# Performance work log

Hardware: AMD Instinct MI355X
Metric: run time of the kernel (lower is better)

The kernel has to match this reference:

```python
import jax, jax.numpy as jnp
import numpy as np

N, E = 50000, 800000
NI, NH, NO, NA = 64, 64, 64, 8
C_WEIGHT = 1.0


def psi(p):
    return jnp.sign(p) * jnp.log(jnp.abs(p) + 1.0)


def batchnorm(x, gamma, beta, eps=1e-5):
    # torch BatchNorm1d (training mode): biased variance over the batch dim
    mu = jnp.mean(x, axis=0)
    var = jnp.var(x, axis=0)
    return (x - mu) / jnp.sqrt(var + eps) * gamma + beta


def setup_inputs() -> dict:
    key = jax.random.key(0)
    ks = jax.random.split(key, 16)
    f32 = jnp.float32

    def w(k, shape, s):
        return jax.random.normal(k, shape, dtype=f32) * s

    inp = {}
    inp["h"] = jax.random.normal(ks[0], (N, NI), dtype=f32)
    inp["x"] = jax.random.normal(ks[1], (N, 4), dtype=f32)
    inp["edge_i"] = jax.random.randint(ks[2], (E,), 0, N)
    inp["edge_j"] = jax.random.randint(ks[3], (E,), 0, N)
    inp["node_attr"] = jax.random.normal(ks[4], (N, NA), dtype=f32)
    # phi_e: Linear(2*NI+2 -> NH, no bias), BN, ReLU, Linear(NH -> NH), ReLU
    inp["W_e1"] = w(ks[5], (2 * NI + 2, NH), 0.1)
    inp["g_e"] = jnp.ones((NH,), f32)
    inp["b_e"] = jnp.zeros((NH,), f32)
    inp["W_e2"] = w(ks[6], (NH, NH), 0.1)
    inp["b_e2"] = jnp.zeros((NH,), f32)
    # phi_m: Linear(NH -> 1), Sigmoid
    inp["W_m"] = w(ks[7], (NH, 1), 0.1)
    inp["b_m"] = jnp.zeros((1,), f32)
    # phi_x: Linear(NH -> NH), ReLU, Linear(NH -> 1, no bias, xavier gain=0.001)
    inp["W_x1"] = w(ks[8], (NH, NH), 0.1)
    inp["b_x1"] = jnp.zeros((NH,), f32)
    inp["W_x2"] = w(ks[9], (NH, 1), 0.0003)
    # phi_h: Linear(NH+NI+NA -> NH), BN, ReLU, Linear(NH -> NO)
    inp["W_h1"] = w(ks[10], (NH + NI + NA, NH), 0.1)
    inp["b_h1"] = jnp.zeros((NH,), f32)
    inp["g_h"] = jnp.ones((NH,), f32)
    inp["b_h"] = jnp.zeros((NH,), f32)
    inp["W_h2"] = w(ks[11], (NH, NO), 0.1)
    inp["b_h2"] = jnp.zeros((NO,), f32)
    return inp


def reference(h, x, edge_i, edge_j, node_attr,
              W_e1, g_e, b_e, W_e2, b_e2,
              W_m, b_m, W_x1, b_x1, W_x2,
              W_h1, b_h1, g_h, b_h, W_h2, b_h2):
    n_nodes = h.shape[0]
    xi = x[edge_i]            # [E, 4]
    xj = x[edge_j]            # [E, 4]
    x_diff = xi - xj
    # Minkowski norm / dot: 2*p0*q0 - sum(p*q)
    psq = x_diff * x_diff
    norms = psi(2.0 * psq[:, 0] - psq.sum(axis=-1))[:, None]   # [E,1]
    pq = xi * xj
    dots = psi(2.0 * pq[:, 0] - pq.sum(axis=-1))[:, None]      # [E,1]
    # m_model
    feat = jnp.concatenate([h[edge_i], h[edge_j], norms, dots], axis=1)  # [E, 2*NI+2]
    out = jax.nn.relu(batchnorm(feat @ W_e1, g_e, b_e))
    out = jax.nn.relu(out @ W_e2 + b_e2)
    w_gate = jax.nn.sigmoid(out @ W_m + b_m)
    m = out * w_gate                                            # [E, NH]
    # x_model
    phx = jax.nn.relu(m @ W_x1 + b_x1) @ W_x2                   # [E, 1]
    trans = jnp.clip(x_diff * phx, -100.0, 100.0)
    agg_x = jax.ops.segment_sum(trans, edge_i, num_segments=n_nodes)
    cnt = jax.ops.segment_sum(jnp.ones((trans.shape[0],), trans.dtype),
                              edge_i, num_segments=n_nodes)
    x_new = x + (agg_x / jnp.maximum(cnt, 1.0)[:, None]) * C_WEIGHT
    # h_model
    agg_h = jax.ops.segment_sum(m, edge_i, num_segments=n_nodes)
    hin = jnp.concatenate([h, agg_h, node_attr], axis=1)        # [N, NH+NI+NA]
    hh = jax.nn.relu(batchnorm(hin @ W_h1 + b_h1, g_h, b_h))
    h_new = h + (hh @ W_h2 + b_h2)
    return (h_new, x_new, m)
```

## Files before the change

kernel.cpp:

```cpp
#include <hip/hip_runtime.h>
#include <stdint.h>

typedef __attribute__((ext_vector_type(8))) short bf16x8;
typedef __attribute__((ext_vector_type(4))) float f32x4;

static constexpr int NN = 50000;
static constexpr int NE = 800000;

static constexpr int O_ESUM = 0;
static constexpr int O_ESQ  = 64;
static constexpr int O_HSUM = 128;
static constexpr int O_HSQ  = 192;
static constexpr int O_ESC  = 256;
static constexpr int O_ESH  = 320;
static constexpr int O_HSC  = 384;
static constexpr int O_HSH  = 448;
static constexpr int O_CNT  = 512;
static constexpr int O_ROW  = O_CNT + 50048;
static constexpr int O_CUR  = O_ROW + 50048;
static constexpr int O_BSUM = O_CUR + 50048;
static constexpr int O_CSR  = O_BSUM + 64;
static constexpr int O_PHX  = O_CSR + NE;
static constexpr int O_AGGH = O_PHX + NE;
static constexpr int O_YH   = O_AGGH + NN*64;
static constexpr int O_PQ   = O_YH + NN*64;
static constexpr int O_YB   = O_PQ + NN*64;
static constexpr int O_ND   = O_YB + NE*32;

static constexpr int OUT_X = NN*64;
static constexpr int OUT_M = NN*64 + NN*4;

__device__ __forceinline__ short f2bf(float f){
  uint32_t u = __builtin_bit_cast(uint32_t, f);
  u = (u + 0x7fffu + ((u >> 16) & 1u)) >> 16;
  return (short)u;
}
__device__ __forceinline__ float bflo(uint32_t w){ return __builtin_bit_cast(float, w << 16); }
__device__ __forceinline__ float bfhi(uint32_t w){ return __builtin_bit_cast(float, w & 0xffff0000u); }
__device__ __forceinline__ float psi_f(float p){
  return copysignf(__logf(fabsf(p) + 1.0f), p);
}
__device__ __forceinline__ bf16x8 ldrow8(const float* p){
  float4 p0 = *(const float4*)p;
  float4 p1 = *(const float4*)(p + 4);
  bf16x8 a;
  a[0]=f2bf(p0.x); a[1]=f2bf(p0.y); a[2]=f2bf(p0.z); a[3]=f2bf(p0.w);
  a[4]=f2bf(p1.x); a[5]=f2bf(p1.y); a[6]=f2bf(p1.z); a[7]=f2bf(p1.w);
  return a;
}

__global__ __launch_bounds__(256) void k_pq(
    const float* __restrict__ h, const float* __restrict__ We1,
    ushort* __restrict__ P, ushort* __restrict__ Q)
{
  __shared__ __align__(16) ushort sT[4][1024];
  const int lane = threadIdx.x & 63, wid = threadIdx.x >> 6;
  const int g = lane >> 4, q = lane & 15;
  const int ro = lane >> 2, cb = lane & 3;

  bf16x8 wt[2][4], wm[2][4];
#pragma unroll
  for (int kb=0;kb<2;kb++)
#pragma unroll
    for (int nb=0;nb<4;nb++)
#pragma unroll
      for (int j=0;j<8;j++){
        wt[kb][nb][j] = f2bf(We1[(32*kb + 8*g + j)*64 + 16*nb + q]);
        wm[kb][nb][j] = f2bf(We1[(64 + 32*kb + 8*g + j)*64 + 16*nb + q]);
      }

  ushort* tb = sT[wid];
  const int gw = blockIdx.x*4 + wid, nw = gridDim.x*4;
  for (int t = gw; t < NN/16; t += nw){
    const int rb = t*16;
    const float* hp = h + (size_t)(rb+q)*64;
    bf16x8 a[2];
    a[0] = ldrow8(hp + 8*g); a[1] = ldrow8(hp + 32 + 8*g);

    f32x4 accP[4], accQ[4];
#pragma unroll
    for (int nb=0;nb<4;nb++){ accP[nb] = (f32x4){0.f,0.f,0.f,0.f}; accQ[nb] = (f32x4){0.f,0.f,0.f,0.f}; }
#pragma unroll
    for (int kb=0;kb<2;kb++)
#pragma unroll
      for (int nb=0;nb<4;nb++){
        accP[nb] = __builtin_amdgcn_mfma_f32_16x16x32_bf16(a[kb], wt[kb][nb], accP[nb], 0,0,0);
        accQ[nb] = __builtin_amdgcn_mfma_f32_16x16x32_bf16(a[kb], wm[kb][nb], accQ[nb], 0,0,0);
      }

    asm volatile("s_waitcnt lgkmcnt(0)" ::: "memory");
#pragma unroll
    for (int nb=0;nb<4;nb++)
#pragma unroll
      for (int r=0;r<4;r++){
        const int mr = 4*g + r;
        tb[mr*64 + ((16*nb + q) ^ ((mr&7)<<3))] = (ushort)f2bf(accP[nb][r]);
      }
    asm volatile("s_waitcnt lgkmcnt(0)" ::: "memory");
    {
      const int s = ro & 7;
      uint4 c0 = *(const uint4*)(tb + ro*64 + ((cb*16    ) ^ (s<<3)));
      uint4 c1 = *(const uint4*)(tb + ro*64 + ((cb*16 + 8) ^ (s<<3)));
      *(uint4*)(P + (size_t)(rb+ro)*64 + cb*16    ) = c0;
      *(uint4*)(P + (size_t)(rb+ro)*64 + cb*16 + 8) = c1;
    }
    asm volatile("s_waitcnt lgkmcnt(0)" ::: "memory");
#pragma unroll
    for (int nb=0;nb<4;nb++)
#pragma unroll
      for (int r=0;r<4;r++){
        const int mr = 4*g + r;
        tb[mr*64 + ((16*nb + q) ^ ((mr&7)<<3))] = (ushort)f2bf(accQ[nb][r]);
      }
    asm volatile("s_waitcnt lgkmcnt(0)" ::: "memory");
    {
      const int s = ro & 7;
      uint4 c0 = *(const uint4*)(tb + ro*64 + ((cb*16    ) ^ (s<<3)));
      uint4 c1 = *(const uint4*)(tb + ro*64 + ((cb*16 + 8) ^ (s<<3)));
      *(uint4*)(Q + (size_t)(rb+ro)*64 + cb*16    ) = c0;
      *(uint4*)(Q + (size_t)(rb+ro)*64 + cb*16 + 8) = c1;
    }
  }
}

__global__ __launch_bounds__(256) void k_nd(
    const float* __restrict__ x,
    const int* __restrict__ ei, const int* __restrict__ ej,
    float2* __restrict__ nd, int* __restrict__ cnt)
{
  const int stride = gridDim.x*256;
  for (int e = blockIdx.x*256 + threadIdx.x; e < NE; e += stride){
    const int i = ei[e], j = ej[e];
    const float4 xi = *(const float4*)(x + 4*i);
    const float4 xj = *(const float4*)(x + 4*j);
    const float dx=xi.x-xj.x, dy=xi.y-xj.y, dz=xi.z-xj.z, dw=xi.w-xj.w;
    float2 v;
    v.x = psi_f(dx*dx - dy*dy - dz*dz - dw*dw);
    v.y = psi_f(xi.x*xj.x - xi.y*xj.y - xi.z*xj.z - xi.w*xj.w);
    nd[e] = v;
    atomicAdd(cnt + i, 1);
  }
}

__global__ __launch_bounds__(256) void k_e1(
    const ushort* __restrict__ P, const ushort* __restrict__ Q,
    const int* __restrict__ ei, const int* __restrict__ ej,
    const float2* __restrict__ nd,
    const float* __restrict__ We1,
    ushort* __restrict__ yb, float* __restrict__ wsf)
{
  __shared__ float sred[8][64];
  const int lane = threadIdx.x & 63, wid = threadIdx.x >> 6;
  const float wn = We1[128*64 + lane];
  const float wd = We1[129*64 + lane];
  float ssum = 0.f, ssq = 0.f;

  const int gw = blockIdx.x*4 + wid, nw = gridDim.x*4;
  for (int t = gw; t < NE/8; t += nw){
    const int eb = __builtin_amdgcn_readfirstlane(t*8);
    int iv[8], jv[8];
    float nr[8], dt[8];
#pragma unroll
    for (int k=0;k<8;k++){
      iv[k] = ei[eb+k];
      jv[k] = ej[eb+k];
      const float2 v = nd[eb+k];
      nr[k] = v.x; dt[k] = v.y;
    }
    uint32_t pv[8], qv[8];
#pragma unroll
    for (int k=0;k<8;k++) pv[k] = P[(size_t)iv[k]*64 + lane];
#pragma unroll
    for (int k=0;k<8;k++) qv[k] = Q[(size_t)jv[k]*64 + lane];
#pragma unroll
    for (int k=0;k<8;k++){
      const float y = bflo(pv[k]) + bflo(qv[k]) + nr[k]*wn + dt[k]*wd;
      ssum += y; ssq += y*y;
      yb[(size_t)(eb+k)*64 + lane] = (ushort)f2bf(y);
    }
  }
  sred[wid][lane] = ssum;
  sred[4+wid][lane] = ssq;
  __syncthreads();
  if (wid == 0){
    const float s = sred[0][lane]+sred[1][lane]+sred[2][lane]+sred[3][lane];
    const float z = sred[4][lane]+sred[5][lane]+sred[6][lane]+sred[7][lane];
    atomicAdd(wsf + O_ESUM + lane, s);
    atomicAdd(wsf + O_ESQ  + lane, z);
  }
}

__global__ void k_stats(const float* __restrict__ sum, const float* __restrict__ sq,
                        const float* __restrict__ gam, const float* __restrict__ bet,
                        float* __restrict__ scale, float* __restrict__ shift, float invc){
  int t = threadIdx.x;
  float mu = sum[t]*invc;
  float var = sq[t]*invc - mu*mu;
  float rstd = rsqrtf(var + 1e-5f);
  float sc = gam[t]*rstd;
  scale[t] = sc;
  shift[t] = bet[t] - mu*sc;
}

__global__ __launch_bounds__(1024) void k_scan_a(const int* __restrict__ cnt, int* __restrict__ row1,
                                                 int* __restrict__ bsum, int n){
  int v = blockIdx.x*1024 + threadIdx.x;
  int x = (v < n) ? cnt[v] : 0;
  const int lane = threadIdx.x & 63, wid = threadIdx.x >> 6;
#pragma unroll
  for (int d=1; d<64; d<<=1){ int y = __shfl_up(x, d, 64); if (lane >= d) x += y; }
  __shared__ int ws[16];
  if (lane == 63) ws[wid] = x;
  __syncthreads();
  if (wid == 0){
    int s = (lane < 16) ? ws[lane] : 0;
#pragma unroll
    for (int d=1; d<16; d<<=1){ int y = __shfl_up(s, d, 64); if (lane >= d) s += y; }
    if (lane < 16) ws[lane] = s;
  }
  __syncthreads();
  if (wid > 0) x += ws[wid-1];
  if (v < n) row1[v] = x;
  if (threadIdx.x == 1023) bsum[blockIdx.x] = x;
}

__global__ void k_scan_b(int* __restrict__ bsum, int nb){
  int t = threadIdx.x;
  int s = (t < nb) ? bsum[t] : 0;
#pragma unroll
  for (int d=1; d<64; d<<=1){ int y = __shfl_up(s, d, 64); if (t >= d) s += y; }
  if (t < nb) bsum[t] = s;
}

__global__ __launch_bounds__(1024) void k_scan_c(const int* __restrict__ cnt, int* __restrict__ row,
                                                 int* __restrict__ cur, const int* __restrict__ bsum, int n){
  int v = blockIdx.x*1024 + threadIdx.x;
  if (v == 0) row[0] = 0;
  if (v < n){
    int off = (blockIdx.x > 0) ? bsum[blockIdx.x-1] : 0;
    int incl = row[v+1] + off;
    row[v+1] = incl;
    cur[v] = incl - cnt[v];
  }
}

__global__ __launch_bounds__(256) void k_scatter(const int* __restrict__ ei, int* __restrict__ cur,
                                                 int* __restrict__ csr){
  int e = blockIdx.x*256 + threadIdx.x;
  if (e < NE){ int v = ei[e]; int p = atomicAdd(cur + v, 1); csr[p] = e; }
}

__global__ __launch_bounds__(256) void k_e2(
    const ushort* __restrict__ yb,
    const float* __restrict__ We2, const float* __restrict__ be2,
    const float* __restrict__ Wm, const float* __restrict__ bm,
    const float* __restrict__ Wx1, const float* __restrict__ bx1, const float* __restrict__ Wx2,
    const float* __restrict__ wsf, float* __restrict__ outm, float* __restrict__ phx)
{
  __shared__ uint4 sW[1024];
  __shared__ __align__(16) ushort sT[4][1024];

  const int tid = threadIdx.x;
  const int lane = tid & 63, wid = tid >> 6;
  const int g = lane >> 4, q = lane & 15;

  for (int idx = tid; idx < 1024; idx += 256){
    const float* Wsrc = (idx < 512) ? We2 : Wx1;
    const int base = idx & 511;
    const int c = base >> 6, L = base & 63;
    const int kb = c >> 2, nb = c & 3;
    const int Lg = L >> 4, Ln = L & 15;
    uint32_t w[8];
#pragma unroll
    for (int j=0;j<8;j++)
      w[j] = (uint32_t)(uint16_t)f2bf(Wsrc[(32*kb + 8*Lg + j)*64 + 16*nb + Ln]);
    uint4 u;
    u.x = w[0] | (w[1]<<16); u.y = w[2] | (w[3]<<16);
    u.z = w[4] | (w[5]<<16); u.w = w[6] | (w[7]<<16);
    sW[idx] = u;
  }
  __syncthreads();

  float sc2[2][8], sh2[2][8];
#pragma unroll
  for (int kb=0;kb<2;kb++)
#pragma unroll
    for (int j=0;j<8;j++){
      const int ch = 32*kb + 8*g + j;
      sc2[kb][j] = wsf[O_ESC + ch];
      sh2[kb][j] = wsf[O_ESH + ch];
    }
  float vbe2[4], vbx1[4], vwm[4], vwx2[4];
#pragma unroll
  for (int nb=0;nb<4;nb++){
    const int c = 16*nb + q;
    vbe2[nb] = be2[c]; vbx1[nb] = bx1[c];
    vwm[nb] = Wm[c];  vwx2[nb] = Wx2[c];
  }
  const float bmv = bm[0];
  ushort* tb = sT[wid];

  const int gw = blockIdx.x*4 + wid, nw = gridDim.x*4;
  for (int t = gw; t < NE/16; t += nw){
    const int eb = t*16;

    bf16x8 a2[2];
#pragma unroll
    for (int kb=0;kb<2;kb++){
      const uint4 raw = *(const uint4*)(yb + (size_t)(eb+q)*64 + 32*kb + 8*g);
      const uint32_t w[4] = {raw.x, raw.y, raw.z, raw.w};
#pragma unroll
      for (int p2=0;p2<4;p2++){
        float v0 = fmaxf(bflo(w[p2])*sc2[kb][2*p2]   + sh2[kb][2*p2],   0.f);
        float v1 = fmaxf(bfhi(w[p2])*sc2[kb][2*p2+1] + sh2[kb][2*p2+1], 0.f);
        a2[kb][2*p2]   = f2bf(v0);
        a2[kb][2*p2+1] = f2bf(v1);
      }
    }

    f32x4 acc2[4];
#pragma unroll
    for (int nb=0;nb<4;nb++){ acc2[nb][0]=vbe2[nb]; acc2[nb][1]=vbe2[nb]; acc2[nb][2]=vbe2[nb]; acc2[nb][3]=vbe2[nb]; }
#pragma unroll
    for (int kb=0;kb<2;kb++)
#pragma unroll
      for (int nb=0;nb<4;nb++)
        acc2[nb] = __builtin_amdgcn_mfma_f32_16x16x32_bf16(
            a2[kb], __builtin_bit_cast(bf16x8, sW[(kb*4+nb)*64 + lane]), acc2[nb], 0,0,0);

    float o2[4][4];
#pragma unroll
    for (int nb=0;nb<4;nb++)
#pragma unroll
      for (int r=0;r<4;r++)
        o2[nb][r] = fmaxf(acc2[nb][r], 0.f);

    float gate[4];
#pragma unroll
    for (int r=0;r<4;r++){
      float s = o2[0][r]*vwm[0] + o2[1][r]*vwm[1] + o2[2][r]*vwm[2] + o2[3][r]*vwm[3];
      s += __shfl_xor(s,1,64); s += __shfl_xor(s,2,64);
      s += __shfl_xor(s,4,64); s += __shfl_xor(s,8,64);
      gate[r] = 1.f/(1.f + __expf(-(s + bmv)));
    }

    float mv[4][4];
#pragma unroll
    for (int nb=0;nb<4;nb++)
#pragma unroll
      for (int r=0;r<4;r++){
        mv[nb][r] = o2[nb][r]*gate[r];
        outm[(size_t)(eb + 4*g + r)*64 + 16*nb + q] = mv[nb][r];
      }

    asm volatile("s_waitcnt lgkmcnt(0)" ::: "memory");
#pragma unroll
    for (int nb=0;nb<4;nb++)
#pragma unroll
      for (int r=0;r<4;r++){
        const int mr = 4*g + r;
        tb[mr*64 + ((16*nb + q) ^ ((mr&7)<<3))] = (ushort)f2bf(mv[nb][r]);
      }
    asm volatile("s_waitcnt lgkmcnt(0)" ::: "memory");
    bf16x8 a3[2];
#pragma unroll
    for (int kb=0;kb<2;kb++){
      const int k0 = 32*kb + 8*g;
      uint4 uv = *(const uint4*)(tb + q*64 + (k0 ^ ((q&7)<<3)));
      a3[kb] = __builtin_bit_cast(bf16x8, uv);
    }

    f32x4 acc3[4];
#pragma unroll
    for (int nb=0;nb<4;nb++){ acc3[nb][0]=vbx1[nb]; acc3[nb][1]=vbx1[nb]; acc3[nb][2]=vbx1[nb]; acc3[nb][3]=vbx1[nb]; }
#pragma unroll
    for (int kb=0;kb<2;kb++)
#pragma unroll
      for (int nb=0;nb<4;nb++)
        acc3[nb] = __builtin_amdgcn_mfma_f32_16x16x32_bf16(
            a3[kb], __builtin_bit_cast(bf16x8, sW[512 + (kb*4+nb)*64 + lane]), acc3[nb], 0,0,0);

    float pd[4];
#pragma unroll
    for (int r=0;r<4;r++){
      float s = fmaxf(acc3[0][r],0.f)*vwx2[0] + fmaxf(acc3[1][r],0.f)*vwx2[1]
              + fmaxf(acc3[2][r],0.f)*vwx2[2] + fmaxf(acc3[3][r],0.f)*vwx2[3];
      s += __shfl_xor(s,1,64); s += __shfl_xor(s,2,64);
      s += __shfl_xor(s,4,64); s += __shfl_xor(s,8,64);
      pd[r] = s;
    }
    if (q == 0){
#pragma unroll
      for (int r=0;r<4;r++) phx[eb + 4*g + r] = pd[r];
    }
  }
}

__global__ __launch_bounds__(256) void k_agg(
    const float* __restrict__ x, const int* __restrict__ ej,
    const int* __restrict__ row, const int* __restrict__ csr,
    const float* __restrict__ m, const float* __restrict__ phx,
    float* __restrict__ aggh, float* __restrict__ out)
{
  const int lane = threadIdx.x & 63, wid = threadIdx.x >> 6;
  const int comp = lane & 3, eoff = lane >> 2;
  const int gw = blockIdx.x*4 + wid, nw = gridDim.x*4;
  for (int v = gw; v < NN; v += nw){
    const int s  = __builtin_amdgcn_readfirstlane(row[v]);
    const int e1 = __builtin_amdgcn_readfirstlane(row[v+1]);

    float ah = 0.f;
    int p = s;
    for (; p + 8 <= e1; p += 8){
      const int c0=csr[p+0], c1=csr[p+1], c2=csr[p+2], c3=csr[p+3];
      const int c4=csr[p+4], c5=csr[p+5], c6=csr[p+6], c7=csr[p+7];
      const float v0 = m[(size_t)c0*64 + lane];
      const float v1 = m[(size_t)c1*64 + lane];
      const float v2 = m[(size_t)c2*64 + lane];
      const float v3 = m[(size_t)c3*64 + lane];
      const float v4 = m[(size_t)c4*64 + lane];
      const float v5 = m[(size_t)c5*64 + lane];
      const float v6 = m[(size_t)c6*64 + lane];
      const float v7 = m[(size_t)c7*64 + lane];
      ah += ((v0+v1)+(v2+v3)) + ((v4+v5)+(v6+v7));
    }
    for (; p < e1; ++p) ah += m[(size_t)csr[p]*64 + lane];
    aggh[(size_t)v*64 + lane] = ah;

    const float xv = x[4*v + comp];
    float ax = 0.f;
    for (int p2 = s; p2 < e1; p2 += 16){
      const int idx = p2 + eoff;
      if (idx < e1){
        const int e = csr[idx];
        const int j = ej[e];
        float tr = (xv - x[4*j + comp]) * phx[e];
        ax += fminf(fmaxf(tr, -100.f), 100.f);
      }
    }
    ax += __shfl_xor(ax, 4, 64);
    ax += __shfl_xor(ax, 8, 64);
    ax += __shfl_xor(ax,16, 64);
    ax += __shfl_xor(ax,32, 64);
    if (lane < 4){
      const float deg = (float)(e1 - s);
      out[OUT_X + 4*v + lane] = xv + ax / fmaxf(deg, 1.f);
    }
  }
}

__global__ __launch_bounds__(256) void k_h1(
    const float* __restrict__ h, const float* __restrict__ aggh, const float* __restrict__ attr,
    const float* __restrict__ Wh1, float* __restrict__ yh, float* __restrict__ wsf)
{
  const int lane = threadIdx.x & 63, wid = threadIdx.x >> 6;
  const int g = lane >> 4, q = lane & 15;

  bf16x8 wf[4][4];
#pragma unroll
  for (int kb=0;kb<4;kb++)
#pragma unroll
    for (int nb=0;nb<4;nb++)
#pragma unroll
      for (int j=0;j<8;j++)
        wf[kb][nb][j] = f2bf(Wh1[(32*kb + 8*g + j)*64 + 16*nb + q]);
  float wa[8][4];
#pragma unroll
  for (int a8=0;a8<8;a8++)
#pragma unroll
    for (int nb=0;nb<4;nb++)
      wa[a8][nb] = Wh1[(128+a8)*64 + 16*nb + q];

  float ssum[4]={0.f,0.f,0.f,0.f}, ssq[4]={0.f,0.f,0.f,0.f};
  const int gw = blockIdx.x*4 + wid, nw = gridDim.x*4;
  for (int t = gw; t < NN/16; t += nw){
    const int rb = t*16;
    bf16x8 a[4];
    const float* hp = h    + (size_t)(rb+q)*64;
    const float* ap = aggh + (size_t)(rb+q)*64;
    a[0]=ldrow8(hp + 8*g); a[1]=ldrow8(hp + 32 + 8*g);
    a[2]=ldrow8(ap + 8*g); a[3]=ldrow8(ap + 32 + 8*g);

    float at[4][8];
#pragma unroll
    for (int r=0;r<4;r++){
      const float* pp = attr + (size_t)(rb + 4*g + r)*8;
      float4 p0 = *(const float4*)pp; float4 p1 = *(const float4*)(pp + 4);
      at[r][0]=p0.x; at[r][1]=p0.y; at[r][2]=p0.z; at[r][3]=p0.w;
      at[r][4]=p1.x; at[r][5]=p1.y; at[r][6]=p1.z; at[r][7]=p1.w;
    }
    f32x4 acc[4];
#pragma unroll
    for (int nb=0;nb<4;nb++)
#pragma unroll
      for (int r=0;r<4;r++){
        float ci = 0.f;
#pragma unroll
        for (int a8=0;a8<8;a8++) ci += at[r][a8]*wa[a8][nb];
        acc[nb][r] = ci;
      }
#pragma unroll
    for (int kb=0;kb<4;kb++)
#pragma unroll
      for (int nb=0;nb<4;nb++)
        acc[nb] = __builtin_amdgcn_mfma_f32_16x16x32_bf16(a[kb], wf[kb][nb], acc[nb], 0,0,0);

#pragma unroll
    for (int nb=0;nb<4;nb++)
#pragma unroll
      for (int r=0;r<4;r++){
        float v = acc[nb][r];
        yh[(size_t)(rb + 4*g + r)*64 + 16*nb + q] = v;
        ssum[nb] += v; ssq[nb] += v*v;
      }
  }
#pragma unroll
  for (int nb=0;nb<4;nb++){
    float s = ssum[nb], z = ssq[nb];
    s += __shfl_xor(s,16,64); s += __shfl_xor(s,32,64);
    z += __shfl_xor(z,16,64); z += __shfl_xor(z,32,64);
    if (lane < 16){
      atomicAdd(wsf + O_HSUM + 16*nb + lane, s);
      atomicAdd(wsf + O_HSQ  + 16*nb + lane, z);
    }
  }
}

__global__ __launch_bounds__(256) void k_h2(
    const float* __restrict__ h, const float* __restrict__ yh,
    const float* __restrict__ Wh2, const float* __restrict__ bh2,
    const float* __restrict__ wsf, float* __restrict__ out)
{
  const int lane = threadIdx.x & 63, wid = threadIdx.x >> 6;
  const int g = lane >> 4, q = lane & 15;

  bf16x8 wf[2][4];
#pragma unroll
  for (int kb=0;kb<2;kb++)
#pragma unroll
    for (int nb=0;nb<4;nb++)
#pragma unroll
      for (int j=0;j<8;j++)
        wf[kb][nb][j] = f2bf(Wh2[(32*kb + 8*g + j)*64 + 16*nb + q]);

  float sc[2][8], sh[2][8];
#pragma unroll
  for (int kb=0;kb<2;kb++)
#pragma unroll
    for (int j=0;j<8;j++){
      const int k = 32*kb + 8*g + j;
      sc[kb][j] = wsf[O_HSC + k]; sh[kb][j] = wsf[O_HSH + k];
    }
  float vb[4];
#pragma unroll
  for (int nb=0;nb<4;nb++) vb[nb] = bh2[16*nb + q];

  const int gw = blockIdx.x*4 + wid, nw = gridDim.x*4;
  for (int t = gw; t < NN/16; t += nw){
    const int rb = t*16;
    const float* yp = yh + (size_t)(rb+q)*64;
    bf16x8 a[2];
#pragma unroll
    for (int kb=0;kb<2;kb++){
      float4 p0 = *(const float4*)(yp + 32*kb + 8*g);
      float4 p1 = *(const float4*)(yp + 32*kb + 8*g + 4);
      float v[8] = {p0.x,p0.y,p0.z,p0.w,p1.x,p1.y,p1.z,p1.w};
#pragma unroll
      for (int j=0;j<8;j++)
        a[kb][j] = f2bf(fmaxf(v[j]*sc[kb][j] + sh[kb][j], 0.f));
    }
    f32x4 acc[4];
#pragma unroll
    for (int nb=0;nb<4;nb++){ acc[nb][0]=vb[nb]; acc[nb][1]=vb[nb]; acc[nb][2]=vb[nb]; acc[nb][3]=vb[nb]; }
#pragma unroll
    for (int kb=0;kb<2;kb++)
#pragma unroll
      for (int nb=0;nb<4;nb++)
        acc[nb] = __builtin_amdgcn_mfma_f32_16x16x32_bf16(a[kb], wf[kb][nb], acc[nb], 0,0,0);

#pragma unroll
    for (int nb=0;nb<4;nb++)
#pragma unroll
      for (int r=0;r<4;r++){
        const size_t idx = (size_t)(rb + 4*g + r)*64 + 16*nb + q;
        out[idx] = h[idx] + acc[nb][r];
      }
  }
}

extern "C" void kernel_launch(void* const* d_in, const int* in_sizes, int n_in,
                              void* d_out, int out_size, void* d_ws, size_t ws_size,
                              hipStream_t stream){
  const float* h    = (const float*)d_in[0];
  const float* x    = (const float*)d_in[1];
  const int*   ei   = (const int*)d_in[2];
  const int*   ej   = (const int*)d_in[3];
  const float* attr = (const float*)d_in[4];
  const float* We1  = (const float*)d_in[5];
  const float* ge   = (const float*)d_in[6];
  const float* be   = (const float*)d_in[7];
  const float* We2  = (const float*)d_in[8];
  const float* be2  = (const float*)d_in[9];
  const float* Wm   = (const float*)d_in[10];
  const float* bm   = (const float*)d_in[11];
  const float* Wx1  = (const float*)d_in[12];
  const float* bx1  = (const float*)d_in[13];
  const float* Wx2  = (const float*)d_in[14];
  const float* Wh1  = (const float*)d_in[15];
  const float* gh   = (const float*)d_in[17];
  const float* bh   = (const float*)d_in[18];
  const float* Wh2  = (const float*)d_in[19];
  const float* bh2  = (const float*)d_in[20];

  float* out = (float*)d_out;
  float* wsf = (float*)d_ws;
  int*   wsi = (int*)d_ws;
  ushort* P  = (ushort*)(wsf + O_PQ);
  ushort* Q  = P + (size_t)NN*64;
  ushort* yb = (ushort*)(wsf + O_YB);
  float2* nd = (float2*)(wsf + O_ND);

  hipMemsetAsync(wsf + O_ESUM, 0, 256*sizeof(float), stream);
  hipMemsetAsync(wsi + O_CNT, 0, NN*sizeof(int), stream);

  k_pq<<<256,256,0,stream>>>(h, We1, P, Q);
  k_nd<<<2048,256,0,stream>>>(x, ei, ej, nd, wsi+O_CNT);
  k_e1<<<2048,256,0,stream>>>(P, Q, ei, ej, nd, We1, yb, wsf);
  k_stats<<<1,64,0,stream>>>(wsf+O_ESUM, wsf+O_ESQ, ge, be, wsf+O_ESC, wsf+O_ESH, 1.0f/(float)NE);
  k_scan_a<<<49,1024,0,stream>>>(wsi+O_CNT, wsi+O_ROW+1, wsi+O_BSUM, NN);
  k_scan_b<<<1,64,0,stream>>>(wsi+O_BSUM, 49);
  k_scan_c<<<49,1024,0,stream>>>(wsi+O_CNT, wsi+O_ROW, wsi+O_CUR, wsi+O_BSUM, NN);
  k_scatter<<<(NE+255)/256,256,0,stream>>>(ei, wsi+O_CUR, wsi+O_CSR);
  k_e2<<<1024,256,0,stream>>>(yb, We2, be2, Wm, bm, Wx1, bx1, Wx2,
                              wsf, out + OUT_M, wsf + O_PHX);
  k_agg<<<2048,256,0,stream>>>(x, ej, wsi+O_ROW, wsi+O_CSR, out + OUT_M, wsf + O_PHX,
                               wsf + O_AGGH, out);
  k_h1<<<256,256,0,stream>>>(h, wsf + O_AGGH, attr, Wh1, wsf + O_YH, wsf);
  k_stats<<<1,64,0,stream>>>(wsf+O_HSUM, wsf+O_HSQ, gh, bh, wsf+O_HSC, wsf+O_HSH, 1.0f/(float)NN);
  k_h2<<<256,256,0,stream>>>(h, wsf + O_YH, Wh2, bh2, wsf, out);
}
```

Before: 403.6 us.

## Fuse edge-geometry into e1, fold memsets/stats into kernels, single-block scan

The separate k_nd pass and its float2 buffer are removed. k_e1 now computes the Minkowski norm/dot features and the degree atomics itself, one edge per lane, and stages (i, j, norm, dot) records in LDS for the gather loop. The two memsets move into k_pq, and both BN-stat kernels are folded into the prologues of k_e2 and k_h2. The three-kernel CSR scan becomes one single-block serial-chunk scan. Together these cut kernel launches and a round trip of the per-edge buffer through global memory. The trade-off is that the one-block scan serialises about fifty chunks and may be slower than the old multi-block scan.

```diff
diff --git a/kernel.cpp b/kernel.cpp
--- a/kernel.cpp
+++ b/kernel.cpp
@@ -11,21 +11,15 @@
 static constexpr int O_ESQ  = 64;
 static constexpr int O_HSUM = 128;
 static constexpr int O_HSQ  = 192;
-static constexpr int O_ESC  = 256;
-static constexpr int O_ESH  = 320;
-static constexpr int O_HSC  = 384;
-static constexpr int O_HSH  = 448;
 static constexpr int O_CNT  = 512;
 static constexpr int O_ROW  = O_CNT + 50048;
 static constexpr int O_CUR  = O_ROW + 50048;
-static constexpr int O_BSUM = O_CUR + 50048;
-static constexpr int O_CSR  = O_BSUM + 64;
+static constexpr int O_CSR  = O_CUR + 50048;
 static constexpr int O_PHX  = O_CSR + NE;
 static constexpr int O_AGGH = O_PHX + NE;
 static constexpr int O_YH   = O_AGGH + NN*64;
 static constexpr int O_PQ   = O_YH + NN*64;
 static constexpr int O_YB   = O_PQ + NN*64;
-static constexpr int O_ND   = O_YB + NE*32;
 
 static constexpr int OUT_X = NN*64;
 static constexpr int OUT_M = NN*64 + NN*4;
@@ -51,13 +45,16 @@
 
 __global__ __launch_bounds__(256) void k_pq(
     const float* __restrict__ h, const float* __restrict__ We1,
-    ushort* __restrict__ P, ushort* __restrict__ Q)
+    ushort* __restrict__ P, ushort* __restrict__ Q,
+    int* __restrict__ cnt, float* __restrict__ wsf)
 {
   __shared__ __align__(16) ushort sT[4][1024];
   const int lane = threadIdx.x & 63, wid = threadIdx.x >> 6;
   const int g = lane >> 4, q = lane & 15;
   const int ro = lane >> 2, cb = lane & 3;
 
+  if (blockIdx.x == 0 && threadIdx.x < 256) wsf[threadIdx.x] = 0.f;
+
   bf16x8 wt[2][4], wm[2][4];
 #pragma unroll
   for (int kb=0;kb<2;kb++)
@@ -73,6 +70,7 @@
   const int gw = blockIdx.x*4 + wid, nw = gridDim.x*4;
   for (int t = gw; t < NN/16; t += nw){
     const int rb = t*16;
+    if (lane < 16) cnt[rb + lane] = 0;
     const float* hp = h + (size_t)(rb+q)*64;
     bf16x8 a[2];
     a[0] = ldrow8(hp + 8*g); a[1] = ldrow8(hp + 32 + 8*g);
@@ -123,32 +121,13 @@
   }
 }
 
-__global__ __launch_bounds__(256) void k_nd(
-    const float* __restrict__ x,
-    const int* __restrict__ ei, const int* __restrict__ ej,
-    float2* __restrict__ nd, int* __restrict__ cnt)
-{
-  const int stride = gridDim.x*256;
-  for (int e = blockIdx.x*256 + threadIdx.x; e < NE; e += stride){
-    const int i = ei[e], j = ej[e];
-    const float4 xi = *(const float4*)(x + 4*i);
-    const float4 xj = *(const float4*)(x + 4*j);
-    const float dx=xi.x-xj.x, dy=xi.y-xj.y, dz=xi.z-xj.z, dw=xi.w-xj.w;
-    float2 v;
-    v.x = psi_f(dx*dx - dy*dy - dz*dz - dw*dw);
-    v.y = psi_f(xi.x*xj.x - xi.y*xj.y - xi.z*xj.z - xi.w*xj.w);
-    nd[e] = v;
-    atomicAdd(cnt + i, 1);
-  }
-}
-
 __global__ __launch_bounds__(256) void k_e1(
     const ushort* __restrict__ P, const ushort* __restrict__ Q,
     const int* __restrict__ ei, const int* __restrict__ ej,
-    const float2* __restrict__ nd,
-    const float* __restrict__ We1,
-    ushort* __restrict__ yb, float* __restrict__ wsf)
+    const float* __restrict__ x, const float* __restrict__ We1,
+    ushort* __restrict__ yb, float* __restrict__ wsf, int* __restrict__ cnt)
 {
+  __shared__ uint4 sED[4][64];
   __shared__ float sred[8][64];
   const int lane = threadIdx.x & 63, wid = threadIdx.x >> 6;
   const float wn = We1[128*64 + lane];
@@ -156,27 +135,44 @@
   float ssum = 0.f, ssq = 0.f;
 
   const int gw = blockIdx.x*4 + wid, nw = gridDim.x*4;
-  for (int t = gw; t < NE/8; t += nw){
-    const int eb = __builtin_amdgcn_readfirstlane(t*8);
-    int iv[8], jv[8];
-    float nr[8], dt[8];
-#pragma unroll
-    for (int k=0;k<8;k++){
-      iv[k] = ei[eb+k];
-      jv[k] = ej[eb+k];
-      const float2 v = nd[eb+k];
-      nr[k] = v.x; dt[k] = v.y;
-    }
-    uint32_t pv[8], qv[8];
-#pragma unroll
-    for (int k=0;k<8;k++) pv[k] = P[(size_t)iv[k]*64 + lane];
-#pragma unroll
-    for (int k=0;k<8;k++) qv[k] = Q[(size_t)jv[k]*64 + lane];
-#pragma unroll
-    for (int k=0;k<8;k++){
-      const float y = bflo(pv[k]) + bflo(qv[k]) + nr[k]*wn + dt[k]*wd;
-      ssum += y; ssq += y*y;
-      yb[(size_t)(eb+k)*64 + lane] = (ushort)f2bf(y);
+  for (int t = gw; t < NE/64; t += nw){
+    const int eb = t*64;
+    {
+      const int e = eb + lane;
+      const int i = ei[e], j = ej[e];
+      const float4 xi = *(const float4*)(x + 4*i);
+      const float4 xj = *(const float4*)(x + 4*j);
+      const float dx=xi.x-xj.x, dy=xi.y-xj.y, dz=xi.z-xj.z, dw=xi.w-xj.w;
+      const float nrm = psi_f(dx*dx - dy*dy - dz*dz - dw*dw);
+      const float dot = psi_f(xi.x*xj.x - xi.y*xj.y - xi.z*xj.z - xi.w*xj.w);
+      atomicAdd(cnt + i, 1);
+      uint4 rec;
+      rec.x = (uint32_t)i; rec.y = (uint32_t)j;
+      rec.z = __builtin_bit_cast(uint32_t, nrm);
+      rec.w = __builtin_bit_cast(uint32_t, dot);
+      sED[wid][lane] = rec;
+    }
+#pragma unroll 1
+    for (int k8 = 0; k8 < 64; k8 += 8){
+      int iv[8], jv[8]; float nr[8], dt[8];
+#pragma unroll
+      for (int k=0;k<8;k++){
+        const uint4 rec = sED[wid][k8+k];
+        iv[k] = (int)rec.x; jv[k] = (int)rec.y;
+        nr[k] = __builtin_bit_cast(float, rec.z);
+        dt[k] = __builtin_bit_cast(float, rec.w);
+      }
+      uint32_t pv[8], qv[8];
+#pragma unroll
+      for (int k=0;k<8;k++) pv[k] = P[(size_t)iv[k]*64 + lane];
+#pragma unroll
+      for (int k=0;k<8;k++) qv[k] = Q[(size_t)jv[k]*64 + lane];
+#pragma unroll
+      for (int k=0;k<8;k++){
+        const float y = bflo(pv[k]) + bflo(qv[k]) + nr[k]*wn + dt[k]*wd;
+        ssum += y; ssq += y*y;
+        yb[(size_t)(eb+k8+k)*64 + lane] = (ushort)f2bf(y);
+      }
     }
   }
   sred[wid][lane] = ssum;
@@ -190,58 +186,37 @@
   }
 }
 
-__global__ void k_stats(const float* __restrict__ sum, const float* __restrict__ sq,
-                        const float* __restrict__ gam, const float* __restrict__ bet,
-                        float* __restrict__ scale, float* __restrict__ shift, float invc){
-  int t = threadIdx.x;
-  float mu = sum[t]*invc;
-  float var = sq[t]*invc - mu*mu;
-  float rstd = rsqrtf(var + 1e-5f);
-  float sc = gam[t]*rstd;
-  scale[t] = sc;
-  shift[t] = bet[t] - mu*sc;
-}
-
-__global__ __launch_bounds__(1024) void k_scan_a(const int* __restrict__ cnt, int* __restrict__ row1,
-                                                 int* __restrict__ bsum, int n){
-  int v = blockIdx.x*1024 + threadIdx.x;
-  int x = (v < n) ? cnt[v] : 0;
-  const int lane = threadIdx.x & 63, wid = threadIdx.x >> 6;
-#pragma unroll
-  for (int d=1; d<64; d<<=1){ int y = __shfl_up(x, d, 64); if (lane >= d) x += y; }
-  __shared__ int ws[16];
-  if (lane == 63) ws[wid] = x;
-  __syncthreads();
-  if (wid == 0){
-    int s = (lane < 16) ? ws[lane] : 0;
-#pragma unroll
-    for (int d=1; d<16; d<<=1){ int y = __shfl_up(s, d, 64); if (lane >= d) s += y; }
-    if (lane < 16) ws[lane] = s;
-  }
-  __syncthreads();
-  if (wid > 0) x += ws[wid-1];
-  if (v < n) row1[v] = x;
-  if (threadIdx.x == 1023) bsum[blockIdx.x] = x;
-}
-
-__global__ void k_scan_b(int* __restrict__ bsum, int nb){
-  int t = threadIdx.x;
-  int s = (t < nb) ? bsum[t] : 0;
-#pragma unroll
-  for (int d=1; d<64; d<<=1){ int y = __shfl_up(s, d, 64); if (t >= d) s += y; }
-  if (t < nb) bsum[t] = s;
-}
-
-__global__ __launch_bounds__(1024) void k_scan_c(const int* __restrict__ cnt, int* __restrict__ row,
-                                                 int* __restrict__ cur, const int* __restrict__ bsum, int n){
-  int v = blockIdx.x*1024 + threadIdx.x;
-  if (v == 0) row[0] = 0;
-  if (v < n){
-    int off = (blockIdx.x > 0) ? bsum[blockIdx.x-1] : 0;
-    int incl = row[v+1] + off;
-    row[v+1] = incl;
-    cur[v] = incl - cnt[v];
-  }
+__global__ __launch_bounds__(1024) void k_scan(
+    const int* __restrict__ cnt, int* __restrict__ row, int* __restrict__ cur)
+{
+  __shared__ int wtot[16];
+  const int tid = threadIdx.x, lane = tid & 63, wid = tid >> 6;
+  int carry = 0;
+  for (int base = 0; base < NN; base += 1024){
+    const int v = base + tid;
+    const int val = (v < NN) ? cnt[v] : 0;
+    int xs = val;
+#pragma unroll
+    for (int d=1; d<64; d<<=1){ int y = __shfl_up(xs, d, 64); if (lane >= d) xs += y; }
+    if (lane == 63) wtot[wid] = xs;
+    __syncthreads();
+    if (wid == 0){
+      int s = (lane < 16) ? wtot[lane] : 0;
+#pragma unroll
+      for (int d=1; d<16; d<<=1){ int y = __shfl_up(s, d, 64); if (lane >= d) s += y; }
+      if (lane < 16) wtot[lane] = s;
+    }
+    __syncthreads();
+    const int incl = xs + (wid > 0 ? wtot[wid-1] : 0);
+    if (v < NN){
+      const int st = carry + incl - val;
+      row[v] = st; cur[v] = st;
+    }
+    const int ctot = wtot[15];
+    __syncthreads();
+    carry += ctot;
+  }
+  if (tid == 0) row[NN] = carry;
 }
 
 __global__ __launch_bounds__(256) void k_scatter(const int* __restrict__ ei, int* __restrict__ cur,
@@ -252,6 +227,7 @@
 
 __global__ __launch_bounds__(256) void k_e2(
     const ushort* __restrict__ yb,
+    const float* __restrict__ ge, const float* __restrict__ be,
     const float* __restrict__ We2, const float* __restrict__ be2,
     const float* __restrict__ Wm, const float* __restrict__ bm,
     const float* __restrict__ Wx1, const float* __restrict__ bx1, const float* __restrict__ Wx2,
@@ -259,11 +235,19 @@
 {
   __shared__ uint4 sW[1024];
   __shared__ __align__(16) ushort sT[4][1024];
+  __shared__ float sES[64], sEH[64];
 
   const int tid = threadIdx.x;
   const int lane = tid & 63, wid = tid >> 6;
   const int g = lane >> 4, q = lane & 15;
 
+  if (tid < 64){
+    const float mu  = wsf[O_ESUM + tid] * (1.0f/(float)NE);
+    const float var = wsf[O_ESQ  + tid] * (1.0f/(float)NE) - mu*mu;
+    const float sc  = ge[tid] * rsqrtf(var + 1e-5f);
+    sES[tid] = sc;
+    sEH[tid] = be[tid] - mu*sc;
+  }
   for (int idx = tid; idx < 1024; idx += 256){
     const float* Wsrc = (idx < 512) ? We2 : Wx1;
     const int base = idx & 511;
@@ -287,8 +271,8 @@
 #pragma unroll
     for (int j=0;j<8;j++){
       const int ch = 32*kb + 8*g + j;
-      sc2[kb][j] = wsf[O_ESC + ch];
-      sh2[kb][j] = wsf[O_ESH + ch];
+      sc2[kb][j] = sES[ch];
+      sh2[kb][j] = sEH[ch];
     }
   float vbe2[4], vbx1[4], vwm[4], vwx2[4];
 #pragma unroll
@@ -528,11 +512,23 @@
 
 __global__ __launch_bounds__(256) void k_h2(
     const float* __restrict__ h, const float* __restrict__ yh,
+    const float* __restrict__ gh, const float* __restrict__ bh,
     const float* __restrict__ Wh2, const float* __restrict__ bh2,
     const float* __restrict__ wsf, float* __restrict__ out)
 {
-  const int lane = threadIdx.x & 63, wid = threadIdx.x >> 6;
+  __shared__ float sHS[64], sHH[64];
+  const int tid = threadIdx.x;
+  const int lane = tid & 63, wid = tid >> 6;
   const int g = lane >> 4, q = lane & 15;
+
+  if (tid < 64){
+    const float mu  = wsf[O_HSUM + tid] * (1.0f/(float)NN);
+    const float var = wsf[O_HSQ  + tid] * (1.0f/(float)NN) - mu*mu;
+    const float sc  = gh[tid] * rsqrtf(var + 1e-5f);
+    sHS[tid] = sc;
+    sHH[tid] = bh[tid] - mu*sc;
+  }
+  __syncthreads();
 
   bf16x8 wf[2][4];
 #pragma unroll
@@ -549,7 +545,7 @@
 #pragma unroll
     for (int j=0;j<8;j++){
       const int k = 32*kb + 8*g + j;
-      sc[kb][j] = wsf[O_HSC + k]; sh[kb][j] = wsf[O_HSH + k];
+      sc[kb][j] = sHS[k]; sh[kb][j] = sHH[k];
     }
   float vb[4];
 #pragma unroll
@@ -618,24 +614,15 @@
   ushort* P  = (ushort*)(wsf + O_PQ);
   ushort* Q  = P + (size_t)NN*64;
   ushort* yb = (ushort*)(wsf + O_YB);
-  float2* nd = (float2*)(wsf + O_ND);
-
-  hipMemsetAsync(wsf + O_ESUM, 0, 256*sizeof(float), stream);
-  hipMemsetAsync(wsi + O_CNT, 0, NN*sizeof(int), stream);
-
-  k_pq<<<256,256,0,stream>>>(h, We1, P, Q);
-  k_nd<<<2048,256,0,stream>>>(x, ei, ej, nd, wsi+O_CNT);
-  k_e1<<<2048,256,0,stream>>>(P, Q, ei, ej, nd, We1, yb, wsf);
-  k_stats<<<1,64,0,stream>>>(wsf+O_ESUM, wsf+O_ESQ, ge, be, wsf+O_ESC, wsf+O_ESH, 1.0f/(float)NE);
-  k_scan_a<<<49,1024,0,stream>>>(wsi+O_CNT, wsi+O_ROW+1, wsi+O_BSUM, NN);
-  k_scan_b<<<1,64,0,stream>>>(wsi+O_BSUM, 49);
-  k_scan_c<<<49,1024,0,stream>>>(wsi+O_CNT, wsi+O_ROW, wsi+O_CUR, wsi+O_BSUM, NN);
+
+  k_pq<<<256,256,0,stream>>>(h, We1, P, Q, wsi+O_CNT, wsf);
+  k_e1<<<2048,256,0,stream>>>(P, Q, ei, ej, x, We1, yb, wsf, wsi+O_CNT);
+  k_scan<<<1,1024,0,stream>>>(wsi+O_CNT, wsi+O_ROW, wsi+O_CUR);
   k_scatter<<<(NE+255)/256,256,0,stream>>>(ei, wsi+O_CUR, wsi+O_CSR);
-  k_e2<<<1024,256,0,stream>>>(yb, We2, be2, Wm, bm, Wx1, bx1, Wx2,
+  k_e2<<<1024,256,0,stream>>>(yb, ge, be, We2, be2, Wm, bm, Wx1, bx1, Wx2,
                               wsf, out + OUT_M, wsf + O_PHX);
   k_agg<<<2048,256,0,stream>>>(x, ej, wsi+O_ROW, wsi+O_CSR, out + OUT_M, wsf + O_PHX,
                                wsf + O_AGGH, out);
   k_h1<<<256,256,0,stream>>>(h, wsf + O_AGGH, attr, Wh1, wsf + O_YH, wsf);
-  k_stats<<<1,64,0,stream>>>(wsf+O_HSUM, wsf+O_HSQ, gh, bh, wsf+O_HSC, wsf+O_HSH, 1.0f/(float)NN);
-  k_h2<<<256,256,0,stream>>>(h, wsf + O_YH, Wh2, bh2, wsf, out);
-}
+  k_h2<<<256,256,0,stream>>>(h, wsf + O_YH, gh, bh, Wh2, bh2, wsf, out);
+}
```

After: 418.7 us. +3.7%, slower.
